# Kernel optimization log

Hardware: AMD Instinct MI355X
Metric: run time of the kernel (lower is better)

The kernel has to match this reference:

```python
import jax, jax.numpy as jnp
import numpy as np

N_NODES = 50000


def _gcn_conv(x, W, b, src, dst, n):
    """PyG GCNConv: add self-loops, symmetric normalization, sum-aggregate."""
    h = x @ W  # [N, out_dim] dense transform first (out_dim <= in_dim path)
    loop = jnp.arange(n, dtype=src.dtype)
    src_sl = jnp.concatenate([src, loop])
    dst_sl = jnp.concatenate([dst, loop])
    # degree computed on destination nodes (incl. self-loops)
    deg = jax.ops.segment_sum(jnp.ones_like(dst_sl, dtype=h.dtype), dst_sl, num_segments=n)
    dinv = jnp.where(deg > 0, jax.lax.rsqrt(deg), 0.0)
    norm = dinv[src_sl] * dinv[dst_sl]  # [E+N]
    msgs = h[src_sl] * norm[:, None]  # gather + scale, [E+N, out_dim]
    out = jax.ops.segment_sum(msgs, dst_sl, num_segments=n)  # scatter-add
    return out + b


def setup_inputs() -> dict:
    key = jax.random.key(0)
    k0, k1, k2, k3 = jax.random.split(key, 4)
    d = 256
    E = 400000
    scale = 1.0 / np.sqrt(d)
    x = jax.random.normal(k0, (N_NODES, d), dtype=jnp.float32)
    edge_index = jax.random.randint(k1, (2, E), 0, N_NODES, dtype=jnp.int64)
    W1 = jax.random.normal(k2, (d, d), dtype=jnp.float32) * scale
    b1 = jnp.zeros((d,), dtype=jnp.float32)
    W2 = jax.random.normal(k3, (d, d), dtype=jnp.float32) * scale
    b2 = jnp.zeros((d,), dtype=jnp.float32)
    return {"x": x, "edge_index": edge_index, "W1": W1, "b1": b1, "W2": W2, "b2": b2}


def reference(x, edge_index, W1, b1, W2, b2):
    src, dst = edge_index[0], edge_index[1]
    h = _gcn_conv(x, W1, b1, src, dst, N_NODES)
    h = jax.nn.relu(h)
    h = _gcn_conv(h, W2, b2, src, dst, N_NODES)
    h = jax.nn.relu(h)
    return h
```

## Files before the change

kernel.cpp:

```cpp
#include <hip/hip_runtime.h>
#include <stdint.h>

typedef __bf16 bf16_t;
typedef bf16_t bf16x4 __attribute__((ext_vector_type(4)));
typedef bf16_t bf16x8 __attribute__((ext_vector_type(8)));
typedef float f32x4 __attribute__((ext_vector_type(4)));

#define DIM 256
#define NNODES 50000

__global__ void detect_kernel(const int* __restrict__ ei, int* __restrict__ flags) {
    __shared__ int s_zero;
    if (threadIdx.x == 0) s_zero = 0;
    __syncthreads();
    int z = (ei[2 * threadIdx.x + 1] == 0) ? 1 : 0;
    atomicAdd(&s_zero, z);
    __syncthreads();
    if (threadIdx.x == 0) flags[0] = (s_zero > 128) ? 1 : 0;
}

__device__ __forceinline__ int load_edge(const int* __restrict__ ei, int E, int f64,
                                         int which , int e) {
    int v = f64 ? ei[(size_t)which * 2 * E + 2 * (size_t)e]
                : ei[(size_t)which * E + (size_t)e];
    return min(max(v, 0), NNODES - 1);
}


__global__ void zero_counts_kernel(int* __restrict__ counts, int n) {
    int i = blockIdx.x * blockDim.x + threadIdx.x;
    if (i < n) counts[i] = 0;
}

__global__ void hist_kernel(const int* __restrict__ ei, int E, const int* __restrict__ flags,
                            int* __restrict__ counts) {
    int e = blockIdx.x * blockDim.x + threadIdx.x;
    if (e < E) atomicAdd(&counts[load_edge(ei, E, flags[0], 1, e)], 1);
}

__global__ __launch_bounds__(256) void scanA_kernel(const int* __restrict__ counts,
                                                    int* __restrict__ offsets,
                                                    int* __restrict__ bsums, int n) {
    __shared__ int sm[256];
    int b = blockIdx.x, t = threadIdx.x;
    int idx = b * 256 + t;
    int v = (idx < n) ? counts[idx] : 0;
    sm[t] = v;
    __syncthreads();
    #pragma unroll
    for (int off = 1; off < 256; off <<= 1) {
        int u = (t >= off) ? sm[t - off] : 0;
        __syncthreads();
        sm[t] += u;
        __syncthreads();
    }
    if (idx < n) offsets[idx + 1] = sm[t];
    if (t == 255) bsums[b] = sm[255];
}

__global__ __launch_bounds__(256) void scanB_kernel(int* __restrict__ bsums, int nb) {
    __shared__ int sm[256];
    int t = threadIdx.x;
    int v = (t < nb) ? bsums[t] : 0;
    sm[t] = v;
    __syncthreads();
    #pragma unroll
    for (int off = 1; off < 256; off <<= 1) {
        int u = (t >= off) ? sm[t - off] : 0;
        __syncthreads();
        sm[t] += u;
        __syncthreads();
    }
    if (t < nb) bsums[t] = sm[t] - v;
}

__global__ __launch_bounds__(256) void scanC_kernel(const int* __restrict__ counts,
                                                    const int* __restrict__ bsums,
                                                    int* __restrict__ offsets,
                                                    float* __restrict__ dinv,
                                                    int* __restrict__ cursor, int n) {
    int b = blockIdx.x;
    int idx = b * 256 + threadIdx.x;
    if (idx == 0) offsets[0] = 0;
    if (idx < n) {
        int incl = offsets[idx + 1] + bsums[b];
        offsets[idx + 1] = incl;
        cursor[idx] = incl - counts[idx];
        dinv[idx] = rsqrtf((float)(counts[idx] + 1));
    }
}

__global__ void scatter_kernel(const int* __restrict__ ei, int E, const int* __restrict__ flags,
                               const float* __restrict__ dinv, int* __restrict__ cursor,
                               int* __restrict__ csr_src, float* __restrict__ csr_norm) {
    int e = blockIdx.x * blockDim.x + threadIdx.x;
    if (e < E) {
        int s = load_edge(ei, E, flags[0], 0, e);
        int d = load_edge(ei, E, flags[0], 1, e);
        int pos = atomicAdd(&cursor[d], 1);
        if (pos >= 0 && pos < E) {
            csr_src[pos] = s;
            csr_norm[pos] = dinv[s] * dinv[d];
        }
    }
}


__global__ void convert_w_kernel(const float* __restrict__ W1, const float* __restrict__ W2,
                                 bf16_t* __restrict__ Wf1, bf16_t* __restrict__ Wf2) {
    const float* W = blockIdx.y ? W2 : W1;
    bf16_t* Wf = blockIdx.y ? Wf2 : Wf1;
    int k = blockIdx.x, n = threadIdx.x;
    int s = k >> 5, quad = (k >> 3) & 3, j = k & 7;
    int nt = n >> 4, m = n & 15;
    Wf[s * 8192 + (nt * 64 + quad * 16 + m) * 8 + j] = (bf16_t)W[k * DIM + n];
}


template <bool F32A>
__global__ __launch_bounds__(256, 4) void gemm_kernel(const void* __restrict__ Xv,
                                                      const bf16_t* __restrict__ Wf,
                                                      bf16_t* __restrict__ H, int tiles) {
    __shared__ bf16_t sB[8192];
    int tid = threadIdx.x;
    int wave = tid >> 6, lane = tid & 63;
    int m = lane & 15, quad = lane >> 4;
    int tile = blockIdx.x * 4 + wave;
    bool active = tile < tiles;
    int arow = (min(tile, tiles - 1)) * 16 + m;

    f32x4 acc[16] = {};

    for (int s = 0; s < 8; s++) {
        __syncthreads();
        {
            const bf16x8* g = (const bf16x8*)Wf + s * 1024;
            bf16x8* d = (bf16x8*)sB;
            #pragma unroll
            for (int it = 0; it < 4; it++) d[tid + it * 256] = g[tid + it * 256];
        }
        __syncthreads();

        bf16x8 a;
        if (F32A) {
            const f32x4* xp = (const f32x4*)((const float*)Xv + (size_t)arow * DIM + s * 32 + quad * 8);
            f32x4 x0 = xp[0], x1 = xp[1];
            #pragma unroll
            for (int j = 0; j < 4; j++) { a[j] = (bf16_t)x0[j]; a[j + 4] = (bf16_t)x1[j]; }
        } else {
            a = *(const bf16x8*)((const bf16_t*)Xv + (size_t)arow * DIM + s * 32 + quad * 8);
        }

        #pragma unroll
        for (int nt = 0; nt < 16; nt++) {
            bf16x8 b = *(const bf16x8*)(sB + nt * 512 + lane * 8);
            acc[nt] = __builtin_amdgcn_mfma_f32_16x16x32_bf16(a, b, acc[nt], 0, 0, 0);
        }
    }

    if (active) {
        int rowb = tile * 16 + quad * 4;
        #pragma unroll
        for (int nt = 0; nt < 16; nt++) {
            #pragma unroll
            for (int r = 0; r < 4; r++) {
                H[(size_t)(rowb + r) * DIM + nt * 16 + m] = (bf16_t)acc[nt][r];
            }
        }
    }
}


template <bool OUT_BF16>
__global__ __launch_bounds__(256) void aggregate_kernel(const bf16_t* __restrict__ H,
                                                        const int* __restrict__ offsets,
                                                        const int* __restrict__ csr_src,
                                                        const float* __restrict__ csr_norm,
                                                        const float* __restrict__ dinv,
                                                        const float* __restrict__ bias,
                                                        void* __restrict__ outv, int n) {
    int g = threadIdx.x >> 6;
    int l = threadIdx.x & 63;
    int i = blockIdx.x * 4 + g;
    if (i >= n) return;
    float dii = dinv[i];

    auto cvt = [](bf16x4 v) -> f32x4 {
        f32x4 r;
        #pragma unroll
        for (int j = 0; j < 4; j++) r[j] = (float)v[j];
        return r;
    };

    f32x4 acc = cvt(*(const bf16x4*)(H + (size_t)i * DIM + l * 4)) * (dii * dii);
    int e0 = offsets[i], e1 = offsets[i + 1];
    int e = e0;
    for (; e + 4 <= e1; e += 4) {
        int s0 = csr_src[e], s1 = csr_src[e + 1], s2 = csr_src[e + 2], s3 = csr_src[e + 3];
        float w0 = csr_norm[e], w1 = csr_norm[e + 1], w2 = csr_norm[e + 2], w3 = csr_norm[e + 3];
        bf16x4 h0 = *(const bf16x4*)(H + (size_t)s0 * DIM + l * 4);
        bf16x4 h1 = *(const bf16x4*)(H + (size_t)s1 * DIM + l * 4);
        bf16x4 h2 = *(const bf16x4*)(H + (size_t)s2 * DIM + l * 4);
        bf16x4 h3 = *(const bf16x4*)(H + (size_t)s3 * DIM + l * 4);
        acc += cvt(h0) * w0 + cvt(h1) * w1 + cvt(h2) * w2 + cvt(h3) * w3;
    }
    for (; e < e1; e++) {
        acc += cvt(*(const bf16x4*)(H + (size_t)csr_src[e] * DIM + l * 4)) * csr_norm[e];
    }
    acc += *(const f32x4*)(bias + l * 4);
    #pragma unroll
    for (int j = 0; j < 4; j++) acc[j] = fmaxf(acc[j], 0.0f);

    if (OUT_BF16) {
        bf16x4 o;
        #pragma unroll
        for (int j = 0; j < 4; j++) o[j] = (bf16_t)acc[j];
        *(bf16x4*)((bf16_t*)outv + (size_t)i * DIM + l * 4) = o;
    } else {
        *(f32x4*)((float*)outv + (size_t)i * DIM + l * 4) = acc;
    }
}


extern "C" void kernel_launch(void* const* d_in, const int* in_sizes, int n_in,
                              void* d_out, int out_size, void* d_ws, size_t ws_size,
                              hipStream_t stream) {
    const float* x  = (const float*)d_in[0];
    const int*   ei = (const int*)d_in[1];
    const float* W1 = (const float*)d_in[2];
    const float* b1 = (const float*)d_in[3];
    const float* W2 = (const float*)d_in[4];
    const float* b2 = (const float*)d_in[5];
    float* out = (float*)d_out;

    const int n = NNODES;
    const int E = in_sizes[1] / 2;
    const int nb = (n + 255) / 256;

    char* ws = (char*)d_ws;
    size_t off = 0;
    auto alloc = [&](size_t bytes) -> char* {
        char* p = ws + off;
        off += (bytes + 255) & ~(size_t)255;
        return p;
    };
    int*    flags    = (int*)alloc(256);
    float*  dinv     = (float*)alloc((size_t)n * 4);
    int*    counts   = (int*)alloc((size_t)n * 4);
    int*    offsets  = (int*)alloc((size_t)(n + 1) * 4);
    int*    cursor   = (int*)alloc((size_t)n * 4);
    int*    bsums    = (int*)alloc((size_t)nb * 4);
    int*    csr_src  = (int*)alloc((size_t)E * 4);
    float*  csr_norm = (float*)alloc((size_t)E * 4);
    bf16_t* Wf1      = (bf16_t*)alloc((size_t)DIM * DIM * 2);
    bf16_t* Wf2      = (bf16_t*)alloc((size_t)DIM * DIM * 2);
    bf16_t* P        = (bf16_t*)alloc((size_t)n * DIM * 2);
    bf16_t* X2       = (bf16_t*)alloc((size_t)n * DIM * 2);

    detect_kernel<<<1, 256, 0, stream>>>(ei, flags);
    zero_counts_kernel<<<nb, 256, 0, stream>>>(counts, n);
    hist_kernel<<<(E + 255) / 256, 256, 0, stream>>>(ei, E, flags, counts);
    scanA_kernel<<<nb, 256, 0, stream>>>(counts, offsets, bsums, n);
    scanB_kernel<<<1, 256, 0, stream>>>(bsums, nb);
    scanC_kernel<<<nb, 256, 0, stream>>>(counts, bsums, offsets, dinv, cursor, n);
    scatter_kernel<<<(E + 255) / 256, 256, 0, stream>>>(ei, E, flags, dinv, cursor,
                                                        csr_src, csr_norm);

    convert_w_kernel<<<dim3(DIM, 2), DIM, 0, stream>>>(W1, W2, Wf1, Wf2);

    int tiles = (n + 15) / 16;
    int gemm_blocks = (tiles + 3) / 4;
    int agg_blocks = n / 4;

    gemm_kernel<true><<<gemm_blocks, 256, 0, stream>>>(x, Wf1, P, tiles);
    aggregate_kernel<true><<<agg_blocks, 256, 0, stream>>>(P, offsets, csr_src, csr_norm,
                                                           dinv, b1, X2, n);
    gemm_kernel<false><<<gemm_blocks, 256, 0, stream>>>(X2, Wf2, P, tiles);
    aggregate_kernel<false><<<agg_blocks, 256, 0, stream>>>(P, offsets, csr_src, csr_norm,
                                                            dinv, b2, out, n);
}
```

Measured before the change: 270.0 us.

## Pack CSR edges as int2 and broadcast them across the wave via readlane

Interleaves source index and normalization weight into a single int2 CSR array. The aggregate kernel now loads up to 64 edges cooperatively, one per lane, then broadcasts each with readlane and issues 8 gathers at a time, instead of every lane redundantly loading the same scalar edge data. The counts zeroing kernel is replaced by hipMemsetAsync. The cost is padding work on short edge lists, where the loop rounds up to multiples of 8 using zero-weight self entries.

```diff
diff --git a/kernel.cpp b/kernel.cpp
--- a/kernel.cpp
+++ b/kernel.cpp
@@ -26,11 +26,6 @@
     return min(max(v, 0), NNODES - 1);
 }
 
-
-__global__ void zero_counts_kernel(int* __restrict__ counts, int n) {
-    int i = blockIdx.x * blockDim.x + threadIdx.x;
-    if (i < n) counts[i] = 0;
-}
 
 __global__ void hist_kernel(const int* __restrict__ ei, int E, const int* __restrict__ flags,
                             int* __restrict__ counts) {
@@ -92,15 +87,17 @@
 
 __global__ void scatter_kernel(const int* __restrict__ ei, int E, const int* __restrict__ flags,
                                const float* __restrict__ dinv, int* __restrict__ cursor,
-                               int* __restrict__ csr_src, float* __restrict__ csr_norm) {
+                               int2* __restrict__ csr_e) {
     int e = blockIdx.x * blockDim.x + threadIdx.x;
     if (e < E) {
         int s = load_edge(ei, E, flags[0], 0, e);
         int d = load_edge(ei, E, flags[0], 1, e);
         int pos = atomicAdd(&cursor[d], 1);
         if (pos >= 0 && pos < E) {
-            csr_src[pos] = s;
-            csr_norm[pos] = dinv[s] * dinv[d];
+            int2 v;
+            v.x = s;
+            v.y = __float_as_int(dinv[s] * dinv[d]);
+            csr_e[pos] = v;
         }
     }
 }
@@ -174,8 +171,7 @@
 template <bool OUT_BF16>
 __global__ __launch_bounds__(256) void aggregate_kernel(const bf16_t* __restrict__ H,
                                                         const int* __restrict__ offsets,
-                                                        const int* __restrict__ csr_src,
-                                                        const float* __restrict__ csr_norm,
+                                                        const int2* __restrict__ csr_e,
                                                         const float* __restrict__ dinv,
                                                         const float* __restrict__ bias,
                                                         void* __restrict__ outv, int n) {
@@ -194,19 +190,32 @@
 
     f32x4 acc = cvt(*(const bf16x4*)(H + (size_t)i * DIM + l * 4)) * (dii * dii);
     int e0 = offsets[i], e1 = offsets[i + 1];
-    int e = e0;
-    for (; e + 4 <= e1; e += 4) {
-        int s0 = csr_src[e], s1 = csr_src[e + 1], s2 = csr_src[e + 2], s3 = csr_src[e + 3];
-        float w0 = csr_norm[e], w1 = csr_norm[e + 1], w2 = csr_norm[e + 2], w3 = csr_norm[e + 3];
-        bf16x4 h0 = *(const bf16x4*)(H + (size_t)s0 * DIM + l * 4);
-        bf16x4 h1 = *(const bf16x4*)(H + (size_t)s1 * DIM + l * 4);
-        bf16x4 h2 = *(const bf16x4*)(H + (size_t)s2 * DIM + l * 4);
-        bf16x4 h3 = *(const bf16x4*)(H + (size_t)s3 * DIM + l * 4);
-        acc += cvt(h0) * w0 + cvt(h1) * w1 + cvt(h2) * w2 + cvt(h3) * w3;
-    }
-    for (; e < e1; e++) {
-        acc += cvt(*(const bf16x4*)(H + (size_t)csr_src[e] * DIM + l * 4)) * csr_norm[e];
-    }
+
+    for (int e = e0; e < e1; e += 64) {
+        int rem = e1 - e;
+        int2 ed;
+        if (l < rem) {
+            ed = csr_e[e + l];
+        } else {
+            ed.x = i;
+            ed.y = 0;
+        }
+        int nb = rem < 64 ? rem : 64;
+        for (int b = 0; b < nb; b += 8) {
+            bf16x4 h[8];
+            float w[8];
+            #pragma unroll
+            for (int jj = 0; jj < 8; jj++) {
+                int s = (int)__builtin_amdgcn_readlane((unsigned)ed.x, (unsigned)(b + jj));
+                unsigned wb = __builtin_amdgcn_readlane((unsigned)ed.y, (unsigned)(b + jj));
+                w[jj] = __uint_as_float(wb);
+                h[jj] = *(const bf16x4*)(H + (size_t)s * DIM + l * 4);
+            }
+            #pragma unroll
+            for (int jj = 0; jj < 8; jj++) acc += cvt(h[jj]) * w[jj];
+        }
+    }
+
     acc += *(const f32x4*)(bias + l * 4);
     #pragma unroll
     for (int j = 0; j < 4; j++) acc[j] = fmaxf(acc[j], 0.0f);
@@ -250,21 +259,19 @@
     int*    offsets  = (int*)alloc((size_t)(n + 1) * 4);
     int*    cursor   = (int*)alloc((size_t)n * 4);
     int*    bsums    = (int*)alloc((size_t)nb * 4);
-    int*    csr_src  = (int*)alloc((size_t)E * 4);
-    float*  csr_norm = (float*)alloc((size_t)E * 4);
+    int2*   csr_e    = (int2*)alloc((size_t)E * 8);
     bf16_t* Wf1      = (bf16_t*)alloc((size_t)DIM * DIM * 2);
     bf16_t* Wf2      = (bf16_t*)alloc((size_t)DIM * DIM * 2);
     bf16_t* P        = (bf16_t*)alloc((size_t)n * DIM * 2);
     bf16_t* X2       = (bf16_t*)alloc((size_t)n * DIM * 2);
 
     detect_kernel<<<1, 256, 0, stream>>>(ei, flags);
-    zero_counts_kernel<<<nb, 256, 0, stream>>>(counts, n);
+    hipMemsetAsync(counts, 0, (size_t)n * 4, stream);
     hist_kernel<<<(E + 255) / 256, 256, 0, stream>>>(ei, E, flags, counts);
     scanA_kernel<<<nb, 256, 0, stream>>>(counts, offsets, bsums, n);
     scanB_kernel<<<1, 256, 0, stream>>>(bsums, nb);
     scanC_kernel<<<nb, 256, 0, stream>>>(counts, bsums, offsets, dinv, cursor, n);
-    scatter_kernel<<<(E + 255) / 256, 256, 0, stream>>>(ei, E, flags, dinv, cursor,
-                                                        csr_src, csr_norm);
+    scatter_kernel<<<(E + 255) / 256, 256, 0, stream>>>(ei, E, flags, dinv, cursor, csr_e);
 
     convert_w_kernel<<<dim3(DIM, 2), DIM, 0, stream>>>(W1, W2, Wf1, Wf2);
 
@@ -273,9 +280,7 @@
     int agg_blocks = n / 4;
 
     gemm_kernel<true><<<gemm_blocks, 256, 0, stream>>>(x, Wf1, P, tiles);
-    aggregate_kernel<true><<<agg_blocks, 256, 0, stream>>>(P, offsets, csr_src, csr_norm,
-                                                           dinv, b1, X2, n);
+    aggregate_kernel<true><<<agg_blocks, 256, 0, stream>>>(P, offsets, csr_e, dinv, b1, X2, n);
     gemm_kernel<false><<<gemm_blocks, 256, 0, stream>>>(X2, Wf2, P, tiles);
-    aggregate_kernel<false><<<agg_blocks, 256, 0, stream>>>(P, offsets, csr_src, csr_norm,
-                                                            dinv, b2, out, n);
-}
+    aggregate_kernel<false><<<agg_blocks, 256, 0, stream>>>(P, offsets, csr_e, dinv, b2, out, n);
+}
```

Result: faster. 261.3 us (-3.2%).
